# Kernel optimization log

Hardware: AMD Instinct MI355X
Metric: run time of the kernel (lower is better)

The kernel has to match this reference:

```python
import jax, jax.numpy as jnp
import numpy as np

B, T, I = 4, 4096, 1024
E, C = 8, 512
O_TOTAL = 8192
O = O_TOTAL // E  # expert_out_features = 1024


def setup_inputs() -> dict:
    key = jax.random.key(0)
    k1, k2, k3, k4 = jax.random.split(key, 4)
    x = jax.random.normal(k1, (B, T, I), dtype=jnp.float32)
    dispatch_mask = jax.random.uniform(k2, (B, T, E, C), dtype=jnp.float32)
    # nn.Linear(in_features, out_features) weight reshaped to [E, O, I]
    bound = 1.0 / np.sqrt(I)
    weight = jax.random.uniform(k3, (E, O, I), dtype=jnp.float32, minval=-bound, maxval=bound)
    bias = jax.random.uniform(k4, (E, O), dtype=jnp.float32, minval=-bound, maxval=bound)
    return {"x": x, "dispatch_mask": dispatch_mask, "weight": weight, "bias": bias}


def reference(x, dispatch_mask, weight, bias):
    # Two-stage contraction avoids a giant 5D intermediate:
    # 1) gather/combine tokens into expert slots: [b,e,c,i]
    slots = jnp.einsum('bti,btec->beci', x, dispatch_mask)
    # 2) per-expert GEMM: [b,e,c,o]
    expert_outputs = jnp.einsum('beci,eoi->beco', slots, weight)
    expert_outputs = expert_outputs + bias[None, :, None, :]
    return expert_outputs
```

## Files before the change

kernel.cpp:

```cpp
#include <hip/hip_runtime.h>
#include <stdint.h>
#include <stddef.h>

#define B_  4
#define T_  4096
#define I_  1024
#define E_  8
#define C_  512
#define O_  1024
#define EC_ (E_*C_)

typedef __attribute__((ext_vector_type(8))) short bf16x8;
typedef __attribute__((ext_vector_type(4))) float f32x4;
typedef __attribute__((ext_vector_type(4))) unsigned short us4;

__device__ __forceinline__ unsigned short f2bf(float f) {
  unsigned u = __builtin_bit_cast(unsigned, f);
  u += 0x7FFFu + ((u >> 16) & 1u);
  return (unsigned short)(u >> 16);
}

__device__ __forceinline__ void async16(const unsigned short* g, unsigned short* l) {
  __builtin_amdgcn_global_load_lds((const __attribute__((address_space(1))) void*)g,
                                   (__attribute__((address_space(3))) void*)l, 16, 0, 0);
}

template<int R, int CC>
__global__ __launch_bounds__(256) void tcast_kernel(const float* __restrict__ in,
                                                    unsigned short* __restrict__ out) {
  __shared__ float ls[64][68];
  const int tilesPerB = (R/64)*(CC/64);
  const int bx = blockIdx.x;
  const int b  = bx / tilesPerB;
  const int t  = bx % tilesPerB;
  const int tr = t / (CC/64);
  const int tc = t % (CC/64);
  const float* ib = in + (size_t)b * R * CC;
  unsigned short* ob = out + (size_t)b * R * CC;
  const int tid = threadIdx.x;
  const int rr  = tid >> 4;
  const int c4  = (tid & 15) * 4;
  #pragma unroll
  for (int p = 0; p < 4; ++p) {
    const int r = p * 16 + rr;
    float4 v = *(const float4*)&ib[(size_t)(tr*64 + r) * CC + tc*64 + c4];
    *(float4*)&ls[r][c4] = v;
  }
  __syncthreads();
  #pragma unroll
  for (int p = 0; p < 4; ++p) {
    const int c = p * 16 + rr;
    us4 o;
    o.x = f2bf(ls[c4+0][c]);
    o.y = f2bf(ls[c4+1][c]);
    o.z = f2bf(ls[c4+2][c]);
    o.w = f2bf(ls[c4+3][c]);
    *(us4*)&ob[(size_t)(tc*64 + c) * R + tr*64 + c4] = o;
  }
}

__global__ __launch_bounds__(256) void wcvt_kernel(const float* __restrict__ in,
                                                   unsigned short* __restrict__ out, int n4) {
  const int i = blockIdx.x * 256 + threadIdx.x;
  if (i >= n4) return;
  float4 v = ((const float4*)in)[i];
  us4 o; o.x = f2bf(v.x); o.y = f2bf(v.y); o.z = f2bf(v.z); o.w = f2bf(v.w);
  ((us4*)out)[i] = o;
}

template<int EPI>
__device__ __forceinline__ void gemm_core(
    const unsigned short* __restrict__ A, int lda,
    const unsigned short* __restrict__ Bm, int ldb,
    unsigned short* __restrict__ Cb, float* __restrict__ Cf, int ldc,
    const float* __restrict__ bias,
    int K, int m0, int n0) {
  __shared__ __align__(16) unsigned short lsA[128*64];
  __shared__ __align__(16) unsigned short lsB[128*64];
  const int tid    = threadIdx.x;
  const int w      = tid >> 6, l = tid & 63;
  const int lane15 = l & 15,  lgrp = l >> 4;
  const int wm     = (w >> 1) * 64, wn = (w & 1) * 64;
  const int srow   = l >> 3;
  const int scol   = (l & 7) * 8;

  f32x4 acc[4][4] = {};

  for (int kt = 0; kt < K; kt += 64) {
    __syncthreads();
    #pragma unroll
    for (int q = 0; q < 4; ++q) {
      const int blkrow = (w*4 + q) * 8;
      async16(A  + (size_t)(m0 + blkrow + srow) * lda + kt + scol, &lsA[(w*4+q)*512]);
      async16(Bm + (size_t)(n0 + blkrow + srow) * ldb + kt + scol, &lsB[(w*4+q)*512]);
    }
    __syncthreads();
    #pragma unroll
    for (int kk = 0; kk < 64; kk += 32) {
      bf16x8 aF[4], bF[4];
      #pragma unroll
      for (int mi = 0; mi < 4; ++mi)
        aF[mi] = *(const bf16x8*)&lsA[(wm + mi*16 + lane15)*64 + kk + lgrp*8];
      #pragma unroll
      for (int ni = 0; ni < 4; ++ni)
        bF[ni] = *(const bf16x8*)&lsB[(wn + ni*16 + lane15)*64 + kk + lgrp*8];
      #pragma unroll
      for (int mi = 0; mi < 4; ++mi)
        #pragma unroll
        for (int ni = 0; ni < 4; ++ni)
          acc[mi][ni] = __builtin_amdgcn_mfma_f32_16x16x32_bf16(aF[mi], bF[ni], acc[mi][ni], 0, 0, 0);
    }
  }

  if (EPI == 0) {
    #pragma unroll
    for (int mi = 0; mi < 4; ++mi)
      #pragma unroll
      for (int r = 0; r < 4; ++r) {
        const size_t mrow = (size_t)(m0 + wm + mi*16 + lgrp*4 + r);
        #pragma unroll
        for (int ni = 0; ni < 4; ++ni)
          Cb[mrow * ldc + n0 + wn + ni*16 + lane15] = f2bf(acc[mi][ni][r]);
      }
  } else {
    float bv[4];
    #pragma unroll
    for (int ni = 0; ni < 4; ++ni) bv[ni] = bias[n0 + wn + ni*16 + lane15];
    #pragma unroll
    for (int mi = 0; mi < 4; ++mi)
      #pragma unroll
      for (int r = 0; r < 4; ++r) {
        const size_t mrow = (size_t)(m0 + wm + mi*16 + lgrp*4 + r);
        #pragma unroll
        for (int ni = 0; ni < 4; ++ni)
          Cf[mrow * ldc + n0 + wn + ni*16 + lane15] = acc[mi][ni][r] + bv[ni];
      }
  }
}

__global__ __launch_bounds__(256) void gemm1_kernel(const unsigned short* __restrict__ maskT,
                                                    const unsigned short* __restrict__ xT,
                                                    unsigned short* __restrict__ slots) {
  const int bx = blockIdx.x;
  const int b  = bx >> 8;
  const int t  = bx & 255;
  const int tm = t & 31, tn = t >> 5;
  gemm_core<0>(maskT + (size_t)b*EC_*T_, T_,
               xT    + (size_t)b*I_*T_,  T_,
               slots + (size_t)b*EC_*I_, nullptr, I_,
               nullptr, T_, tm*128, tn*128);
}

__global__ __launch_bounds__(256) void gemm2_kernel(const unsigned short* __restrict__ slots,
                                                    const unsigned short* __restrict__ wB,
                                                    const float* __restrict__ bias,
                                                    float* __restrict__ out) {
  const int bx = blockIdx.x;
  const int be = bx >> 5;
  const int e  = be & 7;
  const int t  = bx & 31;
  const int tm = t & 3, tn = t >> 2;
  gemm_core<1>(slots + (size_t)be*C_*I_, I_,
               wB    + (size_t)e*O_*I_,  I_,
               nullptr, out + (size_t)be*C_*O_, O_,
               bias + e*O_, I_, tm*128, tn*128);
}

extern "C" void kernel_launch(void* const* d_in, const int* in_sizes, int n_in,
                              void* d_out, int out_size, void* d_ws, size_t ws_size,
                              hipStream_t stream) {
  const float* x      = (const float*)d_in[0];
  const float* mask   = (const float*)d_in[1];
  const float* weight = (const float*)d_in[2];
  const float* bias   = (const float*)d_in[3];
  float* out = (float*)d_out;

  unsigned short* maskT = (unsigned short*)d_ws;
  unsigned short* xT    = (unsigned short*)((char*)d_ws + 134217728);
  unsigned short* wB    = (unsigned short*)((char*)d_ws + 167772160);
  unsigned short* slots = (unsigned short*)((char*)d_ws + 184549376);

  tcast_kernel<T_, EC_><<<dim3(B_*(T_/64)*(EC_/64)), dim3(256), 0, stream>>>(mask, maskT);
  tcast_kernel<T_, I_ ><<<dim3(B_*(T_/64)*(I_/64)),  dim3(256), 0, stream>>>(x, xT);
  wcvt_kernel<<<dim3((E_*O_*I_/4 + 255)/256), dim3(256), 0, stream>>>(weight, wB, E_*O_*I_/4);
  gemm1_kernel<<<dim3(B_*32*8), dim3(256), 0, stream>>>(maskT, xT, slots);
  gemm2_kernel<<<dim3(B_*E_*4*8), dim3(256), 0, stream>>>(slots, wB, bias, out);
}
```

Baseline: 724.8 us.

## Rewrite GEMM core with 256x256 tiles, double-buffered swizzled LDS, XCD-aware mapping

Replaces the 128x128 single-buffered GEMM core with a 512-thread 256x256 tile that double-buffers A/B in LDS and issues async global-to-LDS loads in half-tile stages interleaved with MFMA phases. LDS columns are XOR-swizzled to avoid bank conflicts, setprio is raised around MFMA bursts, and block indices are remapped so tiles sharing operands land on the same XCD. The aim is to hide load latency and raise operand reuse. In exchange it needs 128KB of LDS and many accumulator registers per thread, and relies on hand-placed waitcnt and barrier ordering that is fragile.

```diff
diff --git a/kernel.cpp b/kernel.cpp
--- a/kernel.cpp
+++ b/kernel.cpp
@@ -24,6 +24,9 @@
   __builtin_amdgcn_global_load_lds((const __attribute__((address_space(1))) void*)g,
                                    (__attribute__((address_space(3))) void*)l, 16, 0, 0);
 }
+
+#define FENCE() asm volatile("" ::: "memory")
+#define BAR()   do { FENCE(); __builtin_amdgcn_s_barrier(); FENCE(); } while (0)
 
 template<int R, int CC>
 __global__ __launch_bounds__(256) void tcast_kernel(const float* __restrict__ in,
@@ -73,97 +76,163 @@
     const unsigned short* __restrict__ A, int lda,
     const unsigned short* __restrict__ Bm, int ldb,
     unsigned short* __restrict__ Cb, float* __restrict__ Cf, int ldc,
-    const float* __restrict__ bias,
-    int K, int m0, int n0) {
-  __shared__ __align__(16) unsigned short lsA[128*64];
-  __shared__ __align__(16) unsigned short lsB[128*64];
-  const int tid    = threadIdx.x;
-  const int w      = tid >> 6, l = tid & 63;
-  const int lane15 = l & 15,  lgrp = l >> 4;
-  const int wm     = (w >> 1) * 64, wn = (w & 1) * 64;
-  const int srow   = l >> 3;
-  const int scol   = (l & 7) * 8;
-
-  f32x4 acc[4][4] = {};
-
-  for (int kt = 0; kt < K; kt += 64) {
-    __syncthreads();
+    const float* __restrict__ bias, int K, int m0, int n0)
+{
+  __shared__ __align__(16) unsigned short lsA[2][256*64];
+  __shared__ __align__(16) unsigned short lsB[2][256*64];
+
+  const int tid  = threadIdx.x;
+  const int w    = tid >> 6;
+  const int l    = tid & 63;
+  const int l15  = l & 15;
+  const int lgrp = l >> 4;
+  const int wm   = (w >> 2) << 7;
+  const int wn   = (w & 3) << 6;
+
+  const int srow = (w << 3) + (l >> 3);
+  const int scol = ((l & 7) ^ (l >> 3)) << 3;
+  const int swz  = (l & 7) << 4;
+  const int colK0 = (lgrp << 4) ^ swz;
+  const int colK1 = colK0 ^ 64;
+
+  f32x4 acc[8][4] = {};
+  bf16x8 aF[4][2], bF[4][2];
+
+#define RD_A(buf, mi, kk) \
+  (*(const bf16x8*)((const char*)&lsA[buf][0] + ((wm + ((mi)<<4) + l15) << 7) + ((kk) ? colK1 : colK0)))
+#define RD_B(buf, ni, kk) \
+  (*(const bf16x8*)((const char*)&lsB[buf][0] + ((wn + ((ni)<<4) + l15) << 7) + ((kk) ? colK1 : colK0)))
+
+#define ST_HALF(dst, OP, ld, rbase, half, ktS) do { \
+  async16((OP) + (size_t)((rbase) + ((half)<<7) + srow) * (ld) + (ktS) + scol, \
+          &(dst)[((((half)<<7) + (w<<3)) << 6)]); \
+  async16((OP) + (size_t)((rbase) + ((half)<<7) + 64 + srow) * (ld) + (ktS) + scol, \
+          &(dst)[((((half)<<7) + 64 + (w<<3)) << 6)]); \
+} while (0)
+
+#define MM(miq, niq) do { \
+  __builtin_amdgcn_s_setprio(1); \
+  _Pragma("unroll") for (int mi = 0; mi < 4; ++mi) \
+  _Pragma("unroll") for (int ni = 0; ni < 2; ++ni) \
+  _Pragma("unroll") for (int kk = 0; kk < 2; ++kk) \
+    acc[(miq)*4+mi][(niq)*2+ni] = __builtin_amdgcn_mfma_f32_16x16x32_bf16( \
+        aF[mi][kk], bF[(niq)*2+ni][kk], acc[(miq)*4+mi][(niq)*2+ni], 0, 0, 0); \
+  __builtin_amdgcn_s_setprio(0); \
+} while (0)
+
+#define WAITLDS() do { \
+  asm volatile("s_waitcnt lgkmcnt(0)" ::: "memory"); \
+  __builtin_amdgcn_sched_barrier(0); \
+} while (0)
+
+#define TILE(buf, k1, k2) do { \
+   \
+  _Pragma("unroll") for (int mi = 0; mi < 4; ++mi) { aF[mi][0] = RD_A(buf, mi, 0); aF[mi][1] = RD_A(buf, mi, 1); } \
+  _Pragma("unroll") for (int ni = 0; ni < 2; ++ni) { bF[ni][0] = RD_B(buf, ni, 0); bF[ni][1] = RD_B(buf, ni, 1); } \
+  ST_HALF(lsA[(buf)^1], A, lda, m0, 1, k1); \
+  BAR(); WAITLDS(); \
+  MM(0, 0); \
+  BAR(); \
+   \
+  _Pragma("unroll") for (int ni = 2; ni < 4; ++ni) { bF[ni][0] = RD_B(buf, ni, 0); bF[ni][1] = RD_B(buf, ni, 1); } \
+  ST_HALF(lsB[(buf)^1], Bm, ldb, n0, 1, k1); \
+  BAR(); WAITLDS(); \
+  MM(0, 1); \
+  BAR(); \
+   \
+  _Pragma("unroll") for (int mi = 0; mi < 4; ++mi) { aF[mi][0] = RD_A(buf, mi+4, 0); aF[mi][1] = RD_A(buf, mi+4, 1); } \
+  ST_HALF(lsB[buf], Bm, ldb, n0, 0, k2); \
+  BAR(); WAITLDS(); \
+  MM(1, 0); \
+  BAR(); \
+   \
+  ST_HALF(lsA[buf], A, lda, m0, 0, k2); \
+  BAR(); \
+  MM(1, 1); \
+  asm volatile("s_waitcnt vmcnt(4)" ::: "memory"); \
+  BAR(); \
+} while (0)
+
+  const int nt = K >> 6;
+  ST_HALF(lsB[0], Bm, ldb, n0, 0, 0);
+  ST_HALF(lsA[0], A,  lda, m0, 0, 0);
+  ST_HALF(lsA[0], A,  lda, m0, 1, 0);
+  ST_HALF(lsB[0], Bm, ldb, n0, 1, 0);
+  ST_HALF(lsB[1], Bm, ldb, n0, 0, 64);
+  ST_HALF(lsA[1], A,  lda, m0, 0, 64);
+  asm volatile("s_waitcnt vmcnt(4)" ::: "memory");
+  BAR();
+
+  for (int j = 0; j < (nt >> 1); ++j) {
+    const int t0 = j << 1;
+    const int k1 = (t0 + 1) << 6;
+    const int k2 = (t0 + 2 < nt) ? (t0 + 2) << 6 : 0;
+    const int k3 = (t0 + 3 < nt) ? (t0 + 3) << 6 : 0;
+    TILE(0, k1, k2);
+    TILE(1, k2, k3);
+  }
+  asm volatile("s_waitcnt vmcnt(0)" ::: "memory");
+
+#undef TILE
+#undef WAITLDS
+#undef MM
+#undef ST_HALF
+#undef RD_B
+#undef RD_A
+
+  if (EPI == 0) {
     #pragma unroll
-    for (int q = 0; q < 4; ++q) {
-      const int blkrow = (w*4 + q) * 8;
-      async16(A  + (size_t)(m0 + blkrow + srow) * lda + kt + scol, &lsA[(w*4+q)*512]);
-      async16(Bm + (size_t)(n0 + blkrow + srow) * ldb + kt + scol, &lsB[(w*4+q)*512]);
-    }
-    __syncthreads();
-    #pragma unroll
-    for (int kk = 0; kk < 64; kk += 32) {
-      bf16x8 aF[4], bF[4];
+    for (int mi = 0; mi < 8; ++mi)
       #pragma unroll
-      for (int mi = 0; mi < 4; ++mi)
-        aF[mi] = *(const bf16x8*)&lsA[(wm + mi*16 + lane15)*64 + kk + lgrp*8];
-      #pragma unroll
-      for (int ni = 0; ni < 4; ++ni)
-        bF[ni] = *(const bf16x8*)&lsB[(wn + ni*16 + lane15)*64 + kk + lgrp*8];
-      #pragma unroll
-      for (int mi = 0; mi < 4; ++mi)
+      for (int r = 0; r < 4; ++r) {
+        const size_t row = (size_t)(m0 + wm + mi*16 + lgrp*4 + r);
         #pragma unroll
         for (int ni = 0; ni < 4; ++ni)
-          acc[mi][ni] = __builtin_amdgcn_mfma_f32_16x16x32_bf16(aF[mi], bF[ni], acc[mi][ni], 0, 0, 0);
-    }
-  }
-
-  if (EPI == 0) {
-    #pragma unroll
-    for (int mi = 0; mi < 4; ++mi)
-      #pragma unroll
-      for (int r = 0; r < 4; ++r) {
-        const size_t mrow = (size_t)(m0 + wm + mi*16 + lgrp*4 + r);
-        #pragma unroll
-        for (int ni = 0; ni < 4; ++ni)
-          Cb[mrow * ldc + n0 + wn + ni*16 + lane15] = f2bf(acc[mi][ni][r]);
+          Cb[row * ldc + n0 + wn + ni*16 + l15] = f2bf(acc[mi][ni][r]);
       }
   } else {
     float bv[4];
     #pragma unroll
-    for (int ni = 0; ni < 4; ++ni) bv[ni] = bias[n0 + wn + ni*16 + lane15];
+    for (int ni = 0; ni < 4; ++ni) bv[ni] = bias[n0 + wn + ni*16 + l15];
     #pragma unroll
-    for (int mi = 0; mi < 4; ++mi)
+    for (int mi = 0; mi < 8; ++mi)
       #pragma unroll
       for (int r = 0; r < 4; ++r) {
-        const size_t mrow = (size_t)(m0 + wm + mi*16 + lgrp*4 + r);
+        const size_t row = (size_t)(m0 + wm + mi*16 + lgrp*4 + r);
         #pragma unroll
         for (int ni = 0; ni < 4; ++ni)
-          Cf[mrow * ldc + n0 + wn + ni*16 + lane15] = acc[mi][ni][r] + bv[ni];
+          Cf[row * ldc + n0 + wn + ni*16 + l15] = acc[mi][ni][r] + bv[ni];
       }
   }
 }
 
-__global__ __launch_bounds__(256) void gemm1_kernel(const unsigned short* __restrict__ maskT,
-                                                    const unsigned short* __restrict__ xT,
-                                                    unsigned short* __restrict__ slots) {
-  const int bx = blockIdx.x;
-  const int b  = bx >> 8;
-  const int t  = bx & 255;
-  const int tm = t & 31, tn = t >> 5;
+__global__ __launch_bounds__(512, 2) void gemm1_kernel(const unsigned short* __restrict__ maskT,
+                                                       const unsigned short* __restrict__ xT,
+                                                       unsigned short* __restrict__ slots) {
+  const int wg  = blockIdx.x;
+  const int xcd = wg & 7, s = wg >> 3;
+  const int tn  = s & 3;
+  const int p   = xcd * 8 + (s >> 2);
+  const int b   = p >> 4, tm = p & 15;
   gemm_core<0>(maskT + (size_t)b*EC_*T_, T_,
                xT    + (size_t)b*I_*T_,  T_,
                slots + (size_t)b*EC_*I_, nullptr, I_,
-               nullptr, T_, tm*128, tn*128);
-}
-
-__global__ __launch_bounds__(256) void gemm2_kernel(const unsigned short* __restrict__ slots,
-                                                    const unsigned short* __restrict__ wB,
-                                                    const float* __restrict__ bias,
-                                                    float* __restrict__ out) {
-  const int bx = blockIdx.x;
-  const int be = bx >> 5;
-  const int e  = be & 7;
-  const int t  = bx & 31;
-  const int tm = t & 3, tn = t >> 2;
+               nullptr, T_, tm*256, tn*256);
+}
+
+__global__ __launch_bounds__(512, 2) void gemm2_kernel(const unsigned short* __restrict__ slots,
+                                                       const unsigned short* __restrict__ wB,
+                                                       const float* __restrict__ bias,
+                                                       float* __restrict__ out) {
+  const int wg  = blockIdx.x;
+  const int xcd = wg & 7, s = wg >> 3;
+  const int be  = xcd * 4 + (s >> 3);
+  const int e   = be & 7;
+  const int tm  = (s >> 2) & 1, tn = s & 3;
   gemm_core<1>(slots + (size_t)be*C_*I_, I_,
                wB    + (size_t)e*O_*I_,  I_,
                nullptr, out + (size_t)be*C_*O_, O_,
-               bias + e*O_, I_, tm*128, tn*128);
+               bias + e*O_, I_, tm*256, tn*256);
 }
 
 extern "C" void kernel_launch(void* const* d_in, const int* in_sizes, int n_in,
@@ -183,6 +252,6 @@
   tcast_kernel<T_, EC_><<<dim3(B_*(T_/64)*(EC_/64)), dim3(256), 0, stream>>>(mask, maskT);
   tcast_kernel<T_, I_ ><<<dim3(B_*(T_/64)*(I_/64)),  dim3(256), 0, stream>>>(x, xT);
   wcvt_kernel<<<dim3((E_*O_*I_/4 + 255)/256), dim3(256), 0, stream>>>(weight, wB, E_*O_*I_/4);
-  gemm1_kernel<<<dim3(B_*32*8), dim3(256), 0, stream>>>(maskT, xT, slots);
-  gemm2_kernel<<<dim3(B_*E_*4*8), dim3(256), 0, stream>>>(slots, wB, bias, out);
-}
+  gemm1_kernel<<<dim3(256), dim3(512), 0, stream>>>(maskT, xT, slots);
+  gemm2_kernel<<<dim3(256), dim3(512), 0, stream>>>(slots, wB, bias, out);
+}
```

Measured after the change: 612.8 us. 1.18x faster.
